# Optimization experiments

Measured on AMD Instinct MI355X. Metric: run time of the kernel, lower is better.

Reference implementation:

```python
import jax, jax.numpy as jnp
import numpy as np

D_MODEL = 1024
N_HEADS = 16
D_K = D_MODEL // N_HEADS
THETA = 10000.0
B, S = 2, 2048


def setup_inputs() -> dict:
    key = jax.random.key(0)
    ks = jax.random.split(key, 5)
    sigma = 2.0 / (D_MODEL + D_MODEL) ** 0.5
    x = jax.random.normal(ks[0], (B, S, D_MODEL), dtype=jnp.float32)
    Wq = jax.random.normal(ks[1], (D_MODEL, D_MODEL), dtype=jnp.float32) * sigma
    Wk = jax.random.normal(ks[2], (D_MODEL, D_MODEL), dtype=jnp.float32) * sigma
    Wv = jax.random.normal(ks[3], (D_MODEL, D_MODEL), dtype=jnp.float32) * sigma
    Wo = jax.random.normal(ks[4], (D_MODEL, D_MODEL), dtype=jnp.float32) * sigma
    token_positions = jnp.arange(S, dtype=jnp.int64 if jax.config.read('jax_enable_x64') else jnp.int32)
    return {"x": x, "Wq": Wq, "Wk": Wk, "Wv": Wv, "Wo": Wo, "token_positions": token_positions}


def _apply_rope(t, token_positions):
    # t: (H, B, S, D_K); token_positions: (S,) broadcasts over leading dims
    half = D_K // 2
    inv_freq = 1.0 / (THETA ** (jnp.arange(0, D_K, 2, dtype=jnp.float32) / D_K))  # (half,)
    ang = token_positions.astype(jnp.float32)[..., None] * inv_freq              # (S, half)
    cos, sin = jnp.cos(ang), jnp.sin(ang)
    t2 = t.reshape(*t.shape[:-1], half, 2)  # interleaved pairs
    o0 = t2[..., 0] * cos - t2[..., 1] * sin
    o1 = t2[..., 0] * sin + t2[..., 1] * cos
    return jnp.stack((o0, o1), axis=-1).reshape(t.shape)


def _split_heads(t):
    # (B, S, D_MODEL) -> (H, B, S, D_K)
    Bb, Ss, _ = t.shape
    return jnp.moveaxis(t.reshape(Bb, Ss, N_HEADS, D_K), 2, 0)


def reference(x, Wq, Wk, Wv, Wo, token_positions):
    Q = _split_heads(jnp.einsum('oi,bsi->bso', Wq, x))
    K = _split_heads(jnp.einsum('oi,bsi->bso', Wk, x))
    V = _split_heads(jnp.einsum('oi,bsi->bso', Wv, x))
    Q = _apply_rope(Q, token_positions)
    K = _apply_rope(K, token_positions)
    scores = jnp.einsum('hbqd,hbkd->hbqk', Q, K) * (D_K ** -0.5)  # (H,B,S,S)
    causal = jnp.tril(jnp.ones((S, S), dtype=bool))
    scores = jnp.where(causal, scores, -jnp.inf)
    attn = jax.nn.softmax(scores, axis=-1)
    out = jnp.einsum('hbqk,hbkd->hbqd', attn, V)  # (H,B,S,D_K)
    out = jnp.moveaxis(out, 0, 2).reshape(x.shape[0], x.shape[1], D_MODEL)
    return jnp.einsum('oi,bsi->bso', Wo, out)
```

## Files before the change

### kernel.cpp

```cpp
#include <hip/hip_runtime.h>

#define DM 1024
#define NH 16
#define DK 64
#define BB 2
#define SS 2048

typedef unsigned short u16;
typedef unsigned int   u32;
typedef __bf16 bf16x8 __attribute__((ext_vector_type(8)));
typedef float  f32x4  __attribute__((ext_vector_type(4)));

__device__ __forceinline__ u16 f2bf(float f){
  u32 u = __float_as_uint(f);
  u32 r = (u + 0x7FFFu + ((u >> 16) & 1u)) >> 16;
  return (u16)r;
}
__device__ __forceinline__ float bf2f(u16 v){ return __uint_as_float(((u32)v) << 16); }

__device__ __forceinline__ u32 cvtpk(float lo, float hi){
  u32 r;
  asm volatile("v_cvt_pk_bf16_f32 %0, %1, %2" : "=v"(r) : "v"(lo), "v"(hi));
  return r;
}

__device__ __forceinline__ void gl16(const void* g, void* l){
  __builtin_amdgcn_global_load_lds((const __attribute__((address_space(1))) u32*)g,
                                   (__attribute__((address_space(3))) u32*)l, 16, 0, 0);
}
__device__ __forceinline__ f32x4 mfma16(bf16x8 a, bf16x8 b, f32x4 c){
  return __builtin_amdgcn_mfma_f32_16x16x32_bf16(a, b, c, 0, 0, 0);
}

__global__ void k_cast(const float* __restrict__ x,  const float* __restrict__ wq,
                       const float* __restrict__ wk, const float* __restrict__ wv,
                       const float* __restrict__ wo, u16* __restrict__ xb,
                       u16* __restrict__ wb, float* __restrict__ tab){
  if (blockIdx.x >= 8192){
    int e = (blockIdx.x - 8192)*256 + threadIdx.x;
    int p = e >> 5, j = e & 31;
    float s, c;
    sincosf((float)p * exp2f(-0.4152410118609203f * (float)j), &s, &c);
    float2 v; v.x = c; v.y = s;
    *(float2*)(tab + e*2) = v;
    return;
  }
  int e = blockIdx.x*1024 + threadIdx.x*4;
  int r = e >> 20;
  const float* s; u16* d; int local;
  if (r < 4){ s = x; d = xb; local = e; }
  else {
    const float* ws[4] = {wq, wk, wv, wo};
    int w = r - 4;
    local = e & 0xFFFFF;
    s = ws[w]; d = wb + ((size_t)w << 20);
  }
  float4 v = *(const float4*)(s + local);
  uint2 t; t.x = cvtpk(v.x, v.y); t.y = cvtpk(v.z, v.w);
  *(uint2*)(d + local) = t;
}

template<bool SWAP>
__device__ __forceinline__ void gemm_core(const u16* __restrict__ A, const u16* __restrict__ Bw,
                                          u16* S, f32x4 (&acc)[4][4]){
  const int tid = threadIdx.x, lane = tid & 63, wid = tid >> 6;
  const int m0 = blockIdx.y * 128, n0 = blockIdx.x * 128;
  const int wm = (wid >> 1) * 64, wn = (wid & 1) * 64;
  const int ql = lane & 15, lg = lane >> 4;

  #define STAGE_G(buf, k0)                                                       \
    _Pragma("unroll")                                                            \
    for (int i = 0; i < 4; i++){                                                 \
      int L = i*4096 + tid*16;                                                   \
      int r_ = L >> 7;                                                           \
      int orig = ((L >> 4) & 7) ^ (r_ & 7);                                      \
      const u16* src = (orig < 4)                                                \
          ? (A  + (size_t)(m0 + r_)*DM + (k0) + orig*8)                          \
          : (Bw + (size_t)(n0 + r_)*DM + (k0) + (orig - 4)*8);                   \
      gl16(src, (char*)(buf) + L);                                               \
    }

  #define COMPUTE_T(buf)                                                         \
    {                                                                            \
      bf16x8 af[4], bfr[4];                                                      \
      _Pragma("unroll")                                                          \
      for (int mi = 0; mi < 4; mi++){                                            \
        int r = wm + mi*16 + ql;                                                 \
        af[mi] = *(const bf16x8*)((char*)(buf) + r*128 + ((lg*16) ^ ((r & 7) << 4))); \
      }                                                                          \
      _Pragma("unroll")                                                          \
      for (int ni = 0; ni < 4; ni++){                                            \
        int r = wn + ni*16 + ql;                                                 \
        bfr[ni] = *(const bf16x8*)((char*)(buf) + r*128 + ((64 + lg*16) ^ ((r & 7) << 4))); \
      }                                                                          \
      __builtin_amdgcn_s_setprio(1);                                             \
      _Pragma("unroll")                                                          \
      for (int mi = 0; mi < 4; mi++)                                             \
        _Pragma("unroll")                                                        \
        for (int ni = 0; ni < 4; ni++)                                           \
          acc[mi][ni] = SWAP ? mfma16(bfr[ni], af[mi], acc[mi][ni])              \
                             : mfma16(af[mi], bfr[ni], acc[mi][ni]);             \
      __builtin_amdgcn_s_setprio(0);                                             \
    }

  char* b0 = (char*)S;
  char* b1 = (char*)S + 16384;
  char* b2 = (char*)S + 32768;

  STAGE_G(b0, 0);
  STAGE_G(b1, 32);

  #pragma unroll 3
  for (int t = 0; t < 30; t++){
    asm volatile("s_waitcnt vmcnt(4)" ::: "memory");
    __builtin_amdgcn_s_barrier();
    STAGE_G(b2, (t+2)*32);
    COMPUTE_T(b0);
    char* tmp = b0; b0 = b1; b1 = b2; b2 = tmp;
  }
  asm volatile("s_waitcnt vmcnt(4)" ::: "memory");
  __builtin_amdgcn_s_barrier();
  COMPUTE_T(b0);
  { char* tmp = b0; b0 = b1; b1 = b2; b2 = tmp; }
  asm volatile("s_waitcnt vmcnt(0)" ::: "memory");
  __builtin_amdgcn_s_barrier();
  COMPUTE_T(b0);

  #undef STAGE_G
  #undef COMPUTE_T
}

__global__ __launch_bounds__(256) void k_gemm_qkv(const u16* __restrict__ xb, const u16* __restrict__ Wb,
                                                  u16* __restrict__ Qb, u16* __restrict__ Kb,
                                                  u16* __restrict__ Vt_g, const int* __restrict__ pos,
                                                  const float* __restrict__ tab){
  __shared__ __align__(16) u16 S[3*8192];
  const int z = blockIdx.z;
  const u16* Bw = Wb + ((size_t)z << 20);
  f32x4 acc[4][4] = {};
  gemm_core<true>(xb, Bw, S, acc);
  const int lane = threadIdx.x & 63, wid = threadIdx.x >> 6;
  const int m0 = blockIdx.y*128 + (wid >> 1)*64, n0 = blockIdx.x*128 + (wid & 1)*64;
  const int ql = lane & 15, lg = lane >> 4;

  if (z == 2){
    #pragma unroll
    for (int mi = 0; mi < 4; mi++){
      const int mrow = m0 + mi*16 + ql;
      const int bq = mrow >> 11, sq = mrow & (SS-1);
      u16* vt = Vt_g + ((size_t)bq*NH*DK)*SS + sq;
      #pragma unroll
      for (int ni = 0; ni < 4; ni++){
        const int nb = n0 + ni*16 + lg*4;
        #pragma unroll
        for (int r = 0; r < 4; r++)
          vt[(size_t)(nb + r)*SS] = f2bf(acc[mi][ni][r]);
      }
    }
    return;
  }

  u16* C = (z == 0) ? Qb : Kb;
  const float4* tab4 = (const float4*)tab;
  #pragma unroll
  for (int mi = 0; mi < 4; mi++){
    const int mrow = m0 + mi*16 + ql;
    const int p = pos[mrow & (SS-1)];
    #pragma unroll
    for (int ni = 0; ni < 4; ni++){
      const int nb = n0 + ni*16 + lg*4;
      float o0 = acc[mi][ni][0], o1 = acc[mi][ni][1];
      float o2 = acc[mi][ni][2], o3 = acc[mi][ni][3];
      int j0 = (nb >> 1) & 31;
      float4 cs = tab4[p*16 + (j0 >> 1)];
      float t0 = o0*cs.x - o1*cs.y, t1 = o0*cs.y + o1*cs.x;
      o0 = t0; o1 = t1;
      t0 = o2*cs.z - o3*cs.w; t1 = o2*cs.w + o3*cs.z;
      o2 = t0; o3 = t1;
      uint2 w; w.x = cvtpk(o0, o1); w.y = cvtpk(o2, o3);
      *(uint2*)(C + (size_t)mrow*DM + nb) = w;
    }
  }
}

__global__ __launch_bounds__(256) void k_gemm_out(const u16* __restrict__ AO, const u16* __restrict__ Wo,
                                                  float* __restrict__ Co){
  __shared__ __align__(16) u16 S[3*8192];
  f32x4 acc[4][4] = {};
  gemm_core<false>(AO, Wo, S, acc);
  const int lane = threadIdx.x & 63, wid = threadIdx.x >> 6;
  const int m0 = blockIdx.y*128 + (wid >> 1)*64, n0 = blockIdx.x*128 + (wid & 1)*64;
  #pragma unroll
  for (int mi = 0; mi < 4; mi++)
    #pragma unroll
    for (int ni = 0; ni < 4; ni++)
      #pragma unroll
      for (int r = 0; r < 4; r++){
        int m = m0 + mi*16 + (lane >> 4)*4 + r;
        int n = n0 + ni*16 + (lane & 15);
        Co[(size_t)m*DM + n] = acc[mi][ni][r];
      }
}

__global__ __launch_bounds__(512) void k_attn(const u16* __restrict__ Q, const u16* __restrict__ K,
                                              const u16* __restrict__ Vt_g, u16* __restrict__ AO){
  __shared__ __align__(16) u16 Ks[3][64*64];
  __shared__ __align__(16) u16 Vt[3][64*64];
  __shared__ __align__(16) u16 Ps[8][16*64];
  const int tid = threadIdx.x, lane = tid & 63, wid = tid >> 6;
  const int b = blockIdx.z, h = blockIdx.y;
  const int qb = b ? (15 - (int)blockIdx.x) : (int)blockIdx.x;
  const int qw = qb*128 + wid*16;
  const size_t base = ((size_t)b*SS)*DM + (size_t)h*DK;
  const size_t vtb  = ((size_t)b*NH + h)*DK*SS;
  const int ql = lane & 15, lg = lane >> 4;
  const int NT = 2*qb + 2;

  const u16* qptr = Q + base + (size_t)(qw + ql)*DM + lg*8;
  bf16x8 qf0 = *(const bf16x8*)(qptr);
  bf16x8 qf1 = *(const bf16x8*)(qptr + 32);

  f32x4 oacc[4] = {};
  float m = -3e38f, lsum = 0.f;
  const float SC = 0.18033688011112042f;
  const float THR = 8.0f / SC;

  const int srow = tid >> 3;
  const int sin = ((tid & 7) * 16) ^ ((srow & 7) << 4);

  #define STAGE_A(bi, t)                                                          \
    {                                                                             \
      const int kn0_ = (t)*64;                                                    \
      gl16(K    + base + (size_t)(kn0_ + srow)*DM + (sin >> 1), (char*)Ks[bi] + tid*16); \
      gl16(Vt_g + vtb  + (size_t)srow*SS + kn0_ + (sin >> 1), (char*)Vt[bi] + tid*16);   \
    }

  STAGE_A(0, 0);
  STAGE_A(1, 1);
  asm volatile("s_waitcnt vmcnt(2)" ::: "memory");
  __builtin_amdgcn_s_barrier();

  int c0 = 0, c1 = 1, c2 = 2;
  for (int kt = 0; kt < NT; kt++){
    const int kv0 = kt*64;
    const bool have2 = (kt + 2 < NT);
    if (have2) STAGE_A(c2, kt + 2);

    const bool active = (kv0 <= qw + 15);
    if (active){
      f32x4 sf[4] = {};
      __builtin_amdgcn_s_setprio(1);
      #pragma unroll
      for (int kk = 0; kk < 2; kk++){
        const int co = kk*64 + lg*16;
        #pragma unroll
        for (int f = 0; f < 4; f++){
          int kvr = f*16 + ql;
          bf16x8 kf = *(const bf16x8*)((const char*)Ks[c0] + ((kvr*128 + co) ^ ((kvr & 7) << 4)));
          sf[f] = mfma16(kf, kk ? qf1 : qf0, sf[f]);
        }
      }
      __builtin_amdgcn_s_setprio(0);

      if (kv0 + 63 > qw){
        const int qa = qw + ql;
        #pragma unroll
        for (int f = 0; f < 4; f++)
          #pragma unroll
          for (int r = 0; r < 4; r++){
            int kva = kv0 + f*16 + lg*4 + r;
            sf[f][r] = (kva <= qa) ? sf[f][r] : -3e38f;
          }
      }

      float mx01 = fmaxf(fmaxf(sf[0][0], sf[0][1]), fmaxf(sf[0][2], sf[0][3]));
      float mx23 = fmaxf(fmaxf(sf[1][0], sf[1][1]), fmaxf(sf[1][2], sf[1][3]));
      float mx45 = fmaxf(fmaxf(sf[2][0], sf[2][1]), fmaxf(sf[2][2], sf[2][3]));
      float mx67 = fmaxf(fmaxf(sf[3][0], sf[3][1]), fmaxf(sf[3][2], sf[3][3]));
      float mx = fmaxf(fmaxf(mx01, mx23), fmaxf(mx45, mx67));

      if (!__all(mx <= m + THR)){
        mx = fmaxf(mx, __shfl_xor(mx, 16));
        mx = fmaxf(mx, __shfl_xor(mx, 32));
        const float mn = fmaxf(m, mx);
        const float alpha = exp2f((m - mn)*SC);
        #pragma unroll
        for (int ni = 0; ni < 4; ni++) oacc[ni] *= alpha;
        lsum *= alpha;
        m = mn;
      }

      const float nms = -m*SC;
      float p[4][4];
      float psum = 0.f;
      #pragma unroll
      for (int f = 0; f < 4; f++)
        #pragma unroll
        for (int r = 0; r < 4; r++){
          p[f][r] = exp2f(fmaf(sf[f][r], SC, nms));
          psum += p[f][r];
        }
      lsum += psum;

      #pragma unroll
      for (int f = 0; f < 4; f++)
        #pragma unroll
        for (int r = 0; r < 4; r += 2){
          int kv = f*16 + lg*4 + r;
          int byteoff = (ql*128 + kv*2) ^ ((ql & 7) << 4);
          *(u32*)((char*)Ps[wid] + byteoff) = cvtpk(p[f][r], p[f][r+1]);
        }

      __builtin_amdgcn_s_setprio(1);
      #pragma unroll
      for (int kk = 0; kk < 2; kk++){
        bf16x8 pf = *(const bf16x8*)((const char*)Ps[wid] +
                      ((ql*128 + kk*64 + lg*16) ^ ((ql & 7) << 4)));
        #pragma unroll
        for (int ni = 0; ni < 4; ni++){
          int d = ni*16 + ql;
          bf16x8 vf = *(const bf16x8*)((const char*)Vt[c0] +
                        ((d*128 + kk*64 + lg*16) ^ ((d & 7) << 4)));
          oacc[ni] = mfma16(vf, pf, oacc[ni]);
        }
      }
      __builtin_amdgcn_s_setprio(0);
    }

    if (kt + 1 < NT){
      if (have2) asm volatile("s_waitcnt vmcnt(2)" ::: "memory");
      else       asm volatile("s_waitcnt vmcnt(0)" ::: "memory");
      __builtin_amdgcn_s_barrier();
    }
    int tmp = c0; c0 = c1; c1 = c2; c2 = tmp;
  }
  #undef STAGE_A

  lsum += __shfl_xor(lsum, 16);
  lsum += __shfl_xor(lsum, 32);
  const float rl = 1.0f / lsum;
  #pragma unroll
  for (int ni = 0; ni < 4; ni++)
    #pragma unroll
    for (int r = 0; r < 4; r += 2){
      int d = ni*16 + lg*4 + r;
      int byteoff = (ql*128 + d*2) ^ ((ql & 7) << 4);
      *(u32*)((char*)Ps[wid] + byteoff) = cvtpk(oacc[ni][r]*rl, oacc[ni][r+1]*rl);
    }
  #pragma unroll
  for (int pass = 0; pass < 2; pass++){
    int qr = pass*8 + (lane >> 3);
    int d0 = (lane & 7)*8;
    bf16x8 row = *(const bf16x8*)((const char*)Ps[wid] + ((qr*128 + d0*2) ^ ((qr & 7) << 4)));
    *(bf16x8*)(AO + base + (size_t)(qw + qr)*DM + d0) = row;
  }
}

extern "C" void kernel_launch(void* const* d_in, const int* in_sizes, int n_in,
                              void* d_out, int out_size, void* d_ws, size_t ws_size,
                              hipStream_t stream){
  const float* x   = (const float*)d_in[0];
  const float* Wq  = (const float*)d_in[1];
  const float* Wk  = (const float*)d_in[2];
  const float* Wv  = (const float*)d_in[3];
  const float* Wo  = (const float*)d_in[4];
  const int*   pos = (const int*)d_in[5];
  float* out = (float*)d_out;

  const size_t NEED = ((size_t)41 << 20);
  if (ws_size < NEED){
    hipMemsetAsync(d_out, 0x7f, (size_t)out_size * sizeof(float), stream);
    return;
  }

  char* ws = (char*)d_ws;
  u16* xb   = (u16*)(ws);
  u16* Wb   = (u16*)(ws + ((size_t)8  << 20));
  u16* Qb   = (u16*)(ws + ((size_t)16 << 20));
  u16* Kb   = (u16*)(ws + ((size_t)24 << 20));
  u16* Vt   = (u16*)(ws + ((size_t)32 << 20));
  float* tab = (float*)(ws + ((size_t)40 << 20));
  u16* AO = xb;

  k_cast<<<8448, 256, 0, stream>>>(x, Wq, Wk, Wv, Wo, xb, Wb, tab);
  k_gemm_qkv<<<dim3(8, 32, 3), 256, 0, stream>>>(xb, Wb, Qb, Kb, Vt, pos, tab);
  k_attn<<<dim3(16, 16, 2), 512, 0, stream>>>(Qb, Kb, Vt, AO);
  k_gemm_out<<<dim3(8, 32), 256, 0, stream>>>(AO, Wb + ((size_t)3 << 20), out);
}
```

Baseline: 122.3 us.

## Use 32x32x16 MFMA in attention with 32 query rows per wave

The attention kernel moves from 16x16x32 to 32x32x16 bf16 MFMA tiles. Each wave now owns 32 query rows, and the block shrinks to 4 waves (256 threads) that still cover 128 queries. K/V staging is rewritten so each thread issues two loads per tile, and the softmax, P-store and output-store layouts follow the 32x32 accumulator layout. The aim is fewer LDS fragment reads per FLOP and fewer cross-lane reductions. The cost is more accumulator registers per wave and fewer waves per block to hide latency.

```diff
diff --git a/kernel.cpp b/kernel.cpp
--- a/kernel.cpp
+++ b/kernel.cpp
@@ -10,6 +10,7 @@
 typedef unsigned int   u32;
 typedef __bf16 bf16x8 __attribute__((ext_vector_type(8)));
 typedef float  f32x4  __attribute__((ext_vector_type(4)));
+typedef float  f32x16 __attribute__((ext_vector_type(16)));
 
 __device__ __forceinline__ u16 f2bf(float f){
   u32 u = __float_as_uint(f);
@@ -30,6 +31,9 @@
 }
 __device__ __forceinline__ f32x4 mfma16(bf16x8 a, bf16x8 b, f32x4 c){
   return __builtin_amdgcn_mfma_f32_16x16x32_bf16(a, b, c, 0, 0, 0);
+}
+__device__ __forceinline__ f32x16 mfma32(bf16x8 a, bf16x8 b, f32x16 c){
+  return __builtin_amdgcn_mfma_f32_32x32x16_bf16(a, b, c, 0, 0, 0);
 }
 
 __global__ void k_cast(const float* __restrict__ x,  const float* __restrict__ wq,
@@ -202,42 +206,47 @@
       }
 }
 
-__global__ __launch_bounds__(512) void k_attn(const u16* __restrict__ Q, const u16* __restrict__ K,
+__global__ __launch_bounds__(256) void k_attn(const u16* __restrict__ Q, const u16* __restrict__ K,
                                               const u16* __restrict__ Vt_g, u16* __restrict__ AO){
   __shared__ __align__(16) u16 Ks[3][64*64];
   __shared__ __align__(16) u16 Vt[3][64*64];
-  __shared__ __align__(16) u16 Ps[8][16*64];
+  __shared__ __align__(16) u16 Ps[4][32*64];
   const int tid = threadIdx.x, lane = tid & 63, wid = tid >> 6;
   const int b = blockIdx.z, h = blockIdx.y;
   const int qb = b ? (15 - (int)blockIdx.x) : (int)blockIdx.x;
-  const int qw = qb*128 + wid*16;
+  const int qw = qb*128 + wid*32;
   const size_t base = ((size_t)b*SS)*DM + (size_t)h*DK;
   const size_t vtb  = ((size_t)b*NH + h)*DK*SS;
-  const int ql = lane & 15, lg = lane >> 4;
+  const int qi = lane & 31, hh = lane >> 5;
   const int NT = 2*qb + 2;
 
-  const u16* qptr = Q + base + (size_t)(qw + ql)*DM + lg*8;
+  const u16* qptr = Q + base + (size_t)(qw + qi)*DM + hh*8;
   bf16x8 qf0 = *(const bf16x8*)(qptr);
-  bf16x8 qf1 = *(const bf16x8*)(qptr + 32);
-
-  f32x4 oacc[4] = {};
+  bf16x8 qf1 = *(const bf16x8*)(qptr + 16);
+  bf16x8 qf2 = *(const bf16x8*)(qptr + 32);
+  bf16x8 qf3 = *(const bf16x8*)(qptr + 48);
+
+  f32x16 oacc0 = {}, oacc1 = {};
   float m = -3e38f, lsum = 0.f;
   const float SC = 0.18033688011112042f;
   const float THR = 8.0f / SC;
 
-  const int srow = tid >> 3;
-  const int sin = ((tid & 7) * 16) ^ ((srow & 7) << 4);
-
   #define STAGE_A(bi, t)                                                          \
     {                                                                             \
       const int kn0_ = (t)*64;                                                    \
-      gl16(K    + base + (size_t)(kn0_ + srow)*DM + (sin >> 1), (char*)Ks[bi] + tid*16); \
-      gl16(Vt_g + vtb  + (size_t)srow*SS + kn0_ + (sin >> 1), (char*)Vt[bi] + tid*16);   \
+      _Pragma("unroll")                                                           \
+      for (int i_ = 0; i_ < 2; i_++){                                             \
+        int L = i_*4096 + tid*16;                                                 \
+        int row_ = L >> 7;                                                        \
+        int inner = (L & 127) ^ ((row_ & 7) << 4);                                \
+        gl16(K    + base + (size_t)(kn0_ + row_)*DM + (inner >> 1), (char*)Ks[bi] + L); \
+        gl16(Vt_g + vtb  + (size_t)row_*SS + kn0_ + (inner >> 1), (char*)Vt[bi] + L);   \
+      }                                                                           \
     }
 
   STAGE_A(0, 0);
   STAGE_A(1, 1);
-  asm volatile("s_waitcnt vmcnt(2)" ::: "memory");
+  asm volatile("s_waitcnt vmcnt(4)" ::: "memory");
   __builtin_amdgcn_s_barrier();
 
   int c0 = 0, c1 = 1, c2 = 2;
@@ -246,89 +255,83 @@
     const bool have2 = (kt + 2 < NT);
     if (have2) STAGE_A(c2, kt + 2);
 
-    const bool active = (kv0 <= qw + 15);
+    const bool active = (kv0 <= qw + 31);
     if (active){
-      f32x4 sf[4] = {};
+      f32x16 sf0 = {}, sf1 = {};
       __builtin_amdgcn_s_setprio(1);
-      #pragma unroll
-      for (int kk = 0; kk < 2; kk++){
-        const int co = kk*64 + lg*16;
+      #define QKSTEP(KK, QF)                                                      \
+        {                                                                         \
+          const int co = (KK)*32 + hh*16;                                         \
+          int ra = qi, rb = 32 + qi;                                              \
+          bf16x8 kfa = *(const bf16x8*)((const char*)Ks[c0] + ((ra*128 + co) ^ ((ra & 7) << 4))); \
+          bf16x8 kfb = *(const bf16x8*)((const char*)Ks[c0] + ((rb*128 + co) ^ ((rb & 7) << 4))); \
+          sf0 = mfma32(kfa, QF, sf0);                                             \
+          sf1 = mfma32(kfb, QF, sf1);                                             \
+        }
+      QKSTEP(0, qf0) QKSTEP(1, qf1) QKSTEP(2, qf2) QKSTEP(3, qf3)
+      #undef QKSTEP
+      __builtin_amdgcn_s_setprio(0);
+
+      if (kv0 + 63 > qw){
+        const int qa = qw + qi;
         #pragma unroll
-        for (int f = 0; f < 4; f++){
-          int kvr = f*16 + ql;
-          bf16x8 kf = *(const bf16x8*)((const char*)Ks[c0] + ((kvr*128 + co) ^ ((kvr & 7) << 4)));
-          sf[f] = mfma16(kf, kk ? qf1 : qf0, sf[f]);
+        for (int r = 0; r < 16; r++){
+          int rowoff = (r & 3) + 8*(r >> 2) + 4*hh;
+          sf0[r] = (kv0 + rowoff      <= qa) ? sf0[r] : -3e38f;
+          sf1[r] = (kv0 + 32 + rowoff <= qa) ? sf1[r] : -3e38f;
         }
       }
-      __builtin_amdgcn_s_setprio(0);
-
-      if (kv0 + 63 > qw){
-        const int qa = qw + ql;
-        #pragma unroll
-        for (int f = 0; f < 4; f++)
-          #pragma unroll
-          for (int r = 0; r < 4; r++){
-            int kva = kv0 + f*16 + lg*4 + r;
-            sf[f][r] = (kva <= qa) ? sf[f][r] : -3e38f;
-          }
-      }
-
-      float mx01 = fmaxf(fmaxf(sf[0][0], sf[0][1]), fmaxf(sf[0][2], sf[0][3]));
-      float mx23 = fmaxf(fmaxf(sf[1][0], sf[1][1]), fmaxf(sf[1][2], sf[1][3]));
-      float mx45 = fmaxf(fmaxf(sf[2][0], sf[2][1]), fmaxf(sf[2][2], sf[2][3]));
-      float mx67 = fmaxf(fmaxf(sf[3][0], sf[3][1]), fmaxf(sf[3][2], sf[3][3]));
-      float mx = fmaxf(fmaxf(mx01, mx23), fmaxf(mx45, mx67));
+
+      float mx = -3e38f;
+      #pragma unroll
+      for (int r = 0; r < 16; r++) mx = fmaxf(mx, fmaxf(sf0[r], sf1[r]));
 
       if (!__all(mx <= m + THR)){
-        mx = fmaxf(mx, __shfl_xor(mx, 16));
         mx = fmaxf(mx, __shfl_xor(mx, 32));
         const float mn = fmaxf(m, mx);
         const float alpha = exp2f((m - mn)*SC);
-        #pragma unroll
-        for (int ni = 0; ni < 4; ni++) oacc[ni] *= alpha;
+        oacc0 *= alpha;
+        oacc1 *= alpha;
         lsum *= alpha;
         m = mn;
       }
 
       const float nms = -m*SC;
-      float p[4][4];
+      float p0[16], p1[16];
       float psum = 0.f;
       #pragma unroll
-      for (int f = 0; f < 4; f++)
-        #pragma unroll
-        for (int r = 0; r < 4; r++){
-          p[f][r] = exp2f(fmaf(sf[f][r], SC, nms));
-          psum += p[f][r];
-        }
+      for (int r = 0; r < 16; r++){
+        p0[r] = exp2f(fmaf(sf0[r], SC, nms));
+        p1[r] = exp2f(fmaf(sf1[r], SC, nms));
+        psum += p0[r] + p1[r];
+      }
       lsum += psum;
 
       #pragma unroll
-      for (int f = 0; f < 4; f++)
-        #pragma unroll
-        for (int r = 0; r < 4; r += 2){
-          int kv = f*16 + lg*4 + r;
-          int byteoff = (ql*128 + kv*2) ^ ((ql & 7) << 4);
-          *(u32*)((char*)Ps[wid] + byteoff) = cvtpk(p[f][r], p[f][r+1]);
-        }
+      for (int w = 0; w < 8; w++){
+        const int pb = (w & 1)*2 + (w >> 1)*8;
+        const int kvb0 = 4*hh + pb;
+        const int kvb1 = 32 + 4*hh + pb;
+        *(u32*)((char*)Ps[wid] + ((qi*128 + kvb0*2) ^ ((qi & 7) << 4))) = cvtpk(p0[2*w], p0[2*w+1]);
+        *(u32*)((char*)Ps[wid] + ((qi*128 + kvb1*2) ^ ((qi & 7) << 4))) = cvtpk(p1[2*w], p1[2*w+1]);
+      }
 
       __builtin_amdgcn_s_setprio(1);
       #pragma unroll
-      for (int kk = 0; kk < 2; kk++){
-        bf16x8 pf = *(const bf16x8*)((const char*)Ps[wid] +
-                      ((ql*128 + kk*64 + lg*16) ^ ((ql & 7) << 4)));
-        #pragma unroll
-        for (int ni = 0; ni < 4; ni++){
-          int d = ni*16 + ql;
-          bf16x8 vf = *(const bf16x8*)((const char*)Vt[c0] +
-                        ((d*128 + kk*64 + lg*16) ^ ((d & 7) << 4)));
-          oacc[ni] = mfma16(vf, pf, oacc[ni]);
-        }
+      for (int kc = 0; kc < 4; kc++){
+        const int co = kc*32 + hh*16;
+        bf16x8 pf = *(const bf16x8*)((const char*)Ps[wid] + ((qi*128 + co) ^ ((qi & 7) << 4)));
+        int da = qi, db = 32 + qi;
+        bf16x8 vfa = *(const bf16x8*)((const char*)Vt[c0] + ((da*128 + co) ^ ((da & 7) << 4)));
+        bf16x8 vfb = *(const bf16x8*)((const char*)Vt[c0] + ((db*128 + co) ^ ((db & 7) << 4)));
+        oacc0 = mfma32(vfa, pf, oacc0);
+        oacc1 = mfma32(vfb, pf, oacc1);
       }
       __builtin_amdgcn_s_setprio(0);
     }
 
     if (kt + 1 < NT){
-      if (have2) asm volatile("s_waitcnt vmcnt(2)" ::: "memory");
+      if (have2) asm volatile("s_waitcnt vmcnt(4)" ::: "memory");
       else       asm volatile("s_waitcnt vmcnt(0)" ::: "memory");
       __builtin_amdgcn_s_barrier();
     }
@@ -336,19 +339,20 @@
   }
   #undef STAGE_A
 
-  lsum += __shfl_xor(lsum, 16);
   lsum += __shfl_xor(lsum, 32);
   const float rl = 1.0f / lsum;
   #pragma unroll
-  for (int ni = 0; ni < 4; ni++)
-    #pragma unroll
-    for (int r = 0; r < 4; r += 2){
-      int d = ni*16 + lg*4 + r;
-      int byteoff = (ql*128 + d*2) ^ ((ql & 7) << 4);
-      *(u32*)((char*)Ps[wid] + byteoff) = cvtpk(oacc[ni][r]*rl, oacc[ni][r+1]*rl);
-    }
+  for (int w = 0; w < 8; w++){
+    const int pb = (w & 1)*2 + (w >> 1)*8;
+    const int db0 = 4*hh + pb;
+    const int db1 = 32 + 4*hh + pb;
+    *(u32*)((char*)Ps[wid] + ((qi*128 + db0*2) ^ ((qi & 7) << 4))) =
+        cvtpk(oacc0[2*w]*rl, oacc0[2*w+1]*rl);
+    *(u32*)((char*)Ps[wid] + ((qi*128 + db1*2) ^ ((qi & 7) << 4))) =
+        cvtpk(oacc1[2*w]*rl, oacc1[2*w+1]*rl);
+  }
   #pragma unroll
-  for (int pass = 0; pass < 2; pass++){
+  for (int pass = 0; pass < 4; pass++){
     int qr = pass*8 + (lane >> 3);
     int d0 = (lane & 7)*8;
     bf16x8 row = *(const bf16x8*)((const char*)Ps[wid] + ((qr*128 + d0*2) ^ ((qr & 7) << 4)));
@@ -384,6 +388,6 @@
 
   k_cast<<<8448, 256, 0, stream>>>(x, Wq, Wk, Wv, Wo, xb, Wb, tab);
   k_gemm_qkv<<<dim3(8, 32, 3), 256, 0, stream>>>(xb, Wb, Qb, Kb, Vt, pos, tab);
-  k_attn<<<dim3(16, 16, 2), 512, 0, stream>>>(Qb, Kb, Vt, AO);
+  k_attn<<<dim3(16, 16, 2), 256, 0, stream>>>(Qb, Kb, Vt, AO);
   k_gemm_out<<<dim3(8, 32), 256, 0, stream>>>(AO, Wb + ((size_t)3 << 20), out);
 }
```

Result: slower. 136.6 us (+11.7%).
